# Kernel optimization log

Hardware: AMD Instinct MI355X
Metric: run time of the kernel (lower is better)

## Reference

```python
import jax, jax.numpy as jnp
import numpy as np

B, S, IN, OUT = 4, 2048, 4096, 4096


def setup_inputs() -> dict:
    key = jax.random.key(0)
    kx, kw, kb = jax.random.split(key, 3)
    x = jax.random.randint(kx, (B, S, IN), -127, 128, dtype=jnp.int8)
    weight = jax.random.randint(kw, (OUT, IN), -127, 128, dtype=jnp.int8)
    # original module initializes bias to zeros(int32); use random int32 to exercise the add
    bias = jax.random.randint(kb, (1, OUT), -1000, 1000, dtype=jnp.int32)
    return {"x": x, "weight": weight, "bias": bias}


def reference(x, weight, bias):
    x_shape = x.shape
    x2 = x.reshape(-1, x_shape[-1])  # [tokens, IN], int8
    # dot_general with preferred_element_type=int32 -> int8 inputs, int32 accumulate
    y = jax.lax.dot_general(
        x2, weight,
        dimension_numbers=(((1,), (1,)), ((), ())),
        preferred_element_type=jnp.int32,
    )  # [tokens, OUT] int32
    y = y + bias  # broadcast [1, OUT] int32
    return y.reshape(*x_shape[:-1], -1)
```

## Files before the change

### kernel.cpp

```cpp
#include <hip/hip_runtime.h>
#include <stdint.h>

#define M_TOT 8192
#define N_TOT 4096
#define K_TOT 4096

typedef int v4i  __attribute__((ext_vector_type(4)));
typedef int v16i __attribute__((ext_vector_type(16)));

__device__ __forceinline__ void gload_lds16(const void* g, void* l) {
    __builtin_amdgcn_global_load_lds(
        (const __attribute__((address_space(1))) unsigned int*)g,
        (__attribute__((address_space(3))) unsigned int*)l,
        16, 0, 0);
}

#define WAIT_V0_L0() __builtin_amdgcn_s_waitcnt(0x0070)
#define WAIT_V0()    __builtin_amdgcn_s_waitcnt(0x0f70)
#define SBAR()       __builtin_amdgcn_s_barrier()
#define SFENCE()     __builtin_amdgcn_sched_barrier(0)

__global__ __launch_bounds__(256) void pack2(
        const int4* __restrict__ xs, int4* __restrict__ xd,
        const int4* __restrict__ ws, int4* __restrict__ wd) {
    const int t = blockIdx.x * 256 + threadIdx.x;
#pragma unroll
    for (int it = 0; it < 6; ++it) {
        const long g = (long)it * 524288 + t;
        const int4* __restrict__ src = (it < 4) ? xs : ws;
        int4* __restrict__ dst       = (it < 4) ? xd : wd;
        const long o = (it < 4) ? g : g - 2097152;
        int4 r;
        int* rp = (int*)&r;
#pragma unroll
        for (int q = 0; q < 4; ++q) {
            const int4 a = src[o * 4 + q];
            rp[q] = (a.x & 255) | ((a.y & 255) << 8) |
                    ((a.z & 255) << 16) | (a.w << 24);
        }
        dst[o] = r;
    }
}

__global__ __launch_bounds__(512, 2) void i8gemm_bias(
        const signed char* __restrict__ x,
        const signed char* __restrict__ w,
        const int* __restrict__ bias,
        int* __restrict__ out) {
    __shared__ __align__(16) signed char la[2][256 * 128];
    __shared__ __align__(16) signed char lb[2][256 * 128];

    const int tid  = threadIdx.x;
    const int lane = tid & 63;
    const int wv   = tid >> 6;
    const int l31  = lane & 31;
    const int kh   = lane >> 5;
    const int wr   = wv >> 2;
    const int wc   = wv & 3;

    const int flat = blockIdx.y * gridDim.x + blockIdx.x;
    const int swz  = (flat & 7) * 64 + (flat >> 3);
    const int bn0  = (swz & 15) * 256;
    const int bm0  = (swz >> 4) * 256;

    int bv[2];
#pragma unroll
    for (int j = 0; j < 2; ++j) bv[j] = bias[bn0 + wc * 64 + j * 32 + l31];
    v16i acc[4][2];
#pragma unroll
    for (int i = 0; i < 4; ++i)
#pragma unroll
        for (int j = 0; j < 2; ++j)
#pragma unroll
            for (int r = 0; r < 16; ++r) acc[i][j][r] = bv[j];

    const int fc = (lane & 7) ^ ((lane >> 3) & 7);
    const signed char* pa = x + (long)(bm0 + wv * 32 + (lane >> 3)) * K_TOT + fc * 16;
    const signed char* pb = w + (long)(bn0 + wv * 32 + (lane >> 3)) * K_TOT + fc * 16;
    const int sdst = wv * 32 * 128;

    const int swr  = l31 & 7;
    const int aoff = (wr * 128 + l31) * 128;
    const int boff = (wc * 64  + l31) * 128;
    const int cs0 = ((0 + kh) ^ swr) * 16;
    const int cs1 = ((2 + kh) ^ swr) * 16;
    const int cs2 = ((4 + kh) ^ swr) * 16;
    const int cs3 = ((6 + kh) ^ swr) * 16;

    signed char* A0 = &la[0][0]; signed char* A1 = &la[1][0];
    signed char* B0 = &lb[0][0]; signed char* B1 = &lb[1][0];

#pragma unroll
    for (int u = 0; u < 4; ++u) {
        gload_lds16(pa + (long)u * 8 * K_TOT, A0 + sdst + u * 1024);
        gload_lds16(pb + (long)u * 8 * K_TOT, B0 + sdst + u * 1024);
    }
    WAIT_V0();
    SBAR();
    SFENCE();

    v4i a0[4], b0[2], a1[4], b1[2];
#pragma unroll
    for (int i = 0; i < 4; ++i) a0[i] = *(const v4i*)(A0 + aoff + i * 4096 + cs0);
#pragma unroll
    for (int j = 0; j < 2; ++j) b0[j] = *(const v4i*)(B0 + boff + j * 4096 + cs0);

    const int NT = K_TOT / 128;
    for (int kt = 0; kt < NT; ++kt) {
        SFENCE();
        if (kt + 1 < NT) {
            const long k0 = (long)(kt + 1) * 128;
#pragma unroll
            for (int u = 0; u < 4; ++u) {
                gload_lds16(pa + k0 + (long)u * 8 * K_TOT, A1 + sdst + u * 1024);
                gload_lds16(pb + k0 + (long)u * 8 * K_TOT, B1 + sdst + u * 1024);
            }
        }
        SFENCE();
#pragma unroll
        for (int i = 0; i < 4; ++i) a1[i] = *(const v4i*)(A0 + aoff + i * 4096 + cs1);
#pragma unroll
        for (int j = 0; j < 2; ++j) b1[j] = *(const v4i*)(B0 + boff + j * 4096 + cs1);
        SFENCE();
        __builtin_amdgcn_s_setprio(1);
#pragma unroll
        for (int i = 0; i < 4; ++i)
#pragma unroll
            for (int j = 0; j < 2; ++j)
                acc[i][j] = __builtin_amdgcn_mfma_i32_32x32x32_i8(
                    a0[i], b0[j], acc[i][j], 0, 0, 0);
        __builtin_amdgcn_s_setprio(0);
        SFENCE();
#pragma unroll
        for (int i = 0; i < 4; ++i) a0[i] = *(const v4i*)(A0 + aoff + i * 4096 + cs2);
#pragma unroll
        for (int j = 0; j < 2; ++j) b0[j] = *(const v4i*)(B0 + boff + j * 4096 + cs2);
        SFENCE();
        __builtin_amdgcn_s_setprio(1);
#pragma unroll
        for (int i = 0; i < 4; ++i)
#pragma unroll
            for (int j = 0; j < 2; ++j)
                acc[i][j] = __builtin_amdgcn_mfma_i32_32x32x32_i8(
                    a1[i], b1[j], acc[i][j], 0, 0, 0);
        __builtin_amdgcn_s_setprio(0);
        SFENCE();
#pragma unroll
        for (int i = 0; i < 4; ++i) a1[i] = *(const v4i*)(A0 + aoff + i * 4096 + cs3);
#pragma unroll
        for (int j = 0; j < 2; ++j) b1[j] = *(const v4i*)(B0 + boff + j * 4096 + cs3);
        SFENCE();
        __builtin_amdgcn_s_setprio(1);
#pragma unroll
        for (int i = 0; i < 4; ++i)
#pragma unroll
            for (int j = 0; j < 2; ++j)
                acc[i][j] = __builtin_amdgcn_mfma_i32_32x32x32_i8(
                    a0[i], b0[j], acc[i][j], 0, 0, 0);
        __builtin_amdgcn_s_setprio(0);
        SFENCE();
        WAIT_V0_L0();
        SFENCE();
        SBAR();
        SFENCE();
        if (kt + 1 < NT) {
#pragma unroll
            for (int i = 0; i < 4; ++i) a0[i] = *(const v4i*)(A1 + aoff + i * 4096 + cs0);
#pragma unroll
            for (int j = 0; j < 2; ++j) b0[j] = *(const v4i*)(B1 + boff + j * 4096 + cs0);
        }
        SFENCE();
        __builtin_amdgcn_s_setprio(1);
#pragma unroll
        for (int i = 0; i < 4; ++i)
#pragma unroll
            for (int j = 0; j < 2; ++j)
                acc[i][j] = __builtin_amdgcn_mfma_i32_32x32x32_i8(
                    a1[i], b1[j], acc[i][j], 0, 0, 0);
        __builtin_amdgcn_s_setprio(0);

        signed char* t;
        t = A0; A0 = A1; A1 = t;
        t = B0; B0 = B1; B1 = t;
    }

#pragma unroll
    for (int i = 0; i < 4; ++i) {
        const int mbase = bm0 + wr * 128 + i * 32 + 4 * kh;
#pragma unroll
        for (int j = 0; j < 2; ++j) {
            const int n = bn0 + wc * 64 + j * 32 + l31;
#pragma unroll
            for (int r = 0; r < 16; ++r) {
                const int m = mbase + (r & 3) + 8 * (r >> 2);
                out[(long)m * N_TOT + n] = acc[i][j][r];
            }
        }
    }
}

extern "C" void kernel_launch(void* const* d_in, const int* in_sizes, int n_in,
                              void* d_out, int out_size, void* d_ws, size_t ws_size,
                              hipStream_t stream) {
    const int* x32  = (const int*)d_in[0];
    const int* w32  = (const int*)d_in[1];
    const int* bias = (const int*)d_in[2];
    int*       out  = (int*)d_out;

    signed char* xp = (signed char*)d_ws;
    signed char* wp = (signed char*)d_ws + (size_t)M_TOT * K_TOT;

    pack2<<<2048, 256, 0, stream>>>((const int4*)x32, (int4*)xp,
                                    (const int4*)w32, (int4*)wp);

    dim3 grid(N_TOT / 256, M_TOT / 256);
    i8gemm_bias<<<grid, 512, 0, stream>>>(xp, wp, bias, out);
}
```

Before: 390.5 us.

## Load B operand directly from global into registers, bypassing LDS

The weight (B) tile is no longer staged through shared memory. Each wave now loads its B fragments straight from global memory into registers, prefetched one k-tile ahead, while A keeps the double-buffered LDS path. This halves LDS use and removes the LDS writes and reads for B, which could allow more blocks per CU. The cost is duplicated global/L2 reads of B across waves, less coalesced per-row loads, and more vector registers held live. The vmcnt waits are adjusted so that only the A LDS loads are waited on before the barrier.

Result: slower. 427.8 us (+9.5%).

```diff
diff --git a/kernel.cpp b/kernel.cpp
--- a/kernel.cpp
+++ b/kernel.cpp
@@ -15,8 +15,9 @@
         16, 0, 0);
 }
 
+#define WAIT_V6_L0() __builtin_amdgcn_s_waitcnt(0x0076)
 #define WAIT_V0_L0() __builtin_amdgcn_s_waitcnt(0x0070)
-#define WAIT_V0()    __builtin_amdgcn_s_waitcnt(0x0f70)
+#define WAIT_V8()    __builtin_amdgcn_s_waitcnt(0x0f78)
 #define SBAR()       __builtin_amdgcn_s_barrier()
 #define SFENCE()     __builtin_amdgcn_sched_barrier(0)
 
@@ -48,7 +49,6 @@
         const int* __restrict__ bias,
         int* __restrict__ out) {
     __shared__ __align__(16) signed char la[2][256 * 128];
-    __shared__ __align__(16) signed char lb[2][256 * 128];
 
     const int tid  = threadIdx.x;
     const int lane = tid & 63;
@@ -76,34 +76,38 @@
 
     const int fc = (lane & 7) ^ ((lane >> 3) & 7);
     const signed char* pa = x + (long)(bm0 + wv * 32 + (lane >> 3)) * K_TOT + fc * 16;
-    const signed char* pb = w + (long)(bn0 + wv * 32 + (lane >> 3)) * K_TOT + fc * 16;
     const int sdst = wv * 32 * 128;
 
     const int swr  = l31 & 7;
     const int aoff = (wr * 128 + l31) * 128;
-    const int boff = (wc * 64  + l31) * 128;
     const int cs0 = ((0 + kh) ^ swr) * 16;
     const int cs1 = ((2 + kh) ^ swr) * 16;
     const int cs2 = ((4 + kh) ^ swr) * 16;
     const int cs3 = ((6 + kh) ^ swr) * 16;
 
+    const signed char* qb0 = w + (long)(bn0 + wc * 64 + l31) * K_TOT + kh * 16;
+    const signed char* qb1 = qb0 + (long)32 * K_TOT;
+
     signed char* A0 = &la[0][0]; signed char* A1 = &la[1][0];
-    signed char* B0 = &lb[0][0]; signed char* B1 = &lb[1][0];
-
-#pragma unroll
-    for (int u = 0; u < 4; ++u) {
+
+#pragma unroll
+    for (int u = 0; u < 4; ++u)
         gload_lds16(pa + (long)u * 8 * K_TOT, A0 + sdst + u * 1024);
-        gload_lds16(pb + (long)u * 8 * K_TOT, B0 + sdst + u * 1024);
-    }
-    WAIT_V0();
+    SFENCE();
+    v4i b0[2], b1[2], b2[2], b3[2];
+    b0[0] = *(const v4i*)(qb0);      b0[1] = *(const v4i*)(qb1);
+    b1[0] = *(const v4i*)(qb0 + 32); b1[1] = *(const v4i*)(qb1 + 32);
+    b2[0] = *(const v4i*)(qb0 + 64); b2[1] = *(const v4i*)(qb1 + 64);
+    b3[0] = *(const v4i*)(qb0 + 96); b3[1] = *(const v4i*)(qb1 + 96);
+    qb0 += 128; qb1 += 128;
+    SFENCE();
+    WAIT_V8();
     SBAR();
     SFENCE();
 
-    v4i a0[4], b0[2], a1[4], b1[2];
+    v4i a0[4], a1[4];
 #pragma unroll
     for (int i = 0; i < 4; ++i) a0[i] = *(const v4i*)(A0 + aoff + i * 4096 + cs0);
-#pragma unroll
-    for (int j = 0; j < 2; ++j) b0[j] = *(const v4i*)(B0 + boff + j * 4096 + cs0);
 
     const int NT = K_TOT / 128;
     for (int kt = 0; kt < NT; ++kt) {
@@ -111,16 +115,12 @@
         if (kt + 1 < NT) {
             const long k0 = (long)(kt + 1) * 128;
 #pragma unroll
-            for (int u = 0; u < 4; ++u) {
+            for (int u = 0; u < 4; ++u)
                 gload_lds16(pa + k0 + (long)u * 8 * K_TOT, A1 + sdst + u * 1024);
-                gload_lds16(pb + k0 + (long)u * 8 * K_TOT, B1 + sdst + u * 1024);
-            }
         }
         SFENCE();
 #pragma unroll
         for (int i = 0; i < 4; ++i) a1[i] = *(const v4i*)(A0 + aoff + i * 4096 + cs1);
-#pragma unroll
-        for (int j = 0; j < 2; ++j) b1[j] = *(const v4i*)(B0 + boff + j * 4096 + cs1);
         SFENCE();
         __builtin_amdgcn_s_setprio(1);
 #pragma unroll
@@ -133,8 +133,6 @@
         SFENCE();
 #pragma unroll
         for (int i = 0; i < 4; ++i) a0[i] = *(const v4i*)(A0 + aoff + i * 4096 + cs2);
-#pragma unroll
-        for (int j = 0; j < 2; ++j) b0[j] = *(const v4i*)(B0 + boff + j * 4096 + cs2);
         SFENCE();
         __builtin_amdgcn_s_setprio(1);
 #pragma unroll
@@ -145,43 +143,51 @@
                     a1[i], b1[j], acc[i][j], 0, 0, 0);
         __builtin_amdgcn_s_setprio(0);
         SFENCE();
+        if (kt + 1 < NT) {
+            b0[0] = *(const v4i*)(qb0);      b0[1] = *(const v4i*)(qb1);
+            b1[0] = *(const v4i*)(qb0 + 32); b1[1] = *(const v4i*)(qb1 + 32);
+        }
+        SFENCE();
 #pragma unroll
         for (int i = 0; i < 4; ++i) a1[i] = *(const v4i*)(A0 + aoff + i * 4096 + cs3);
-#pragma unroll
-        for (int j = 0; j < 2; ++j) b1[j] = *(const v4i*)(B0 + boff + j * 4096 + cs3);
-        SFENCE();
-        __builtin_amdgcn_s_setprio(1);
-#pragma unroll
-        for (int i = 0; i < 4; ++i)
-#pragma unroll
-            for (int j = 0; j < 2; ++j)
-                acc[i][j] = __builtin_amdgcn_mfma_i32_32x32x32_i8(
-                    a0[i], b0[j], acc[i][j], 0, 0, 0);
-        __builtin_amdgcn_s_setprio(0);
-        SFENCE();
-        WAIT_V0_L0();
+        SFENCE();
+        __builtin_amdgcn_s_setprio(1);
+#pragma unroll
+        for (int i = 0; i < 4; ++i)
+#pragma unroll
+            for (int j = 0; j < 2; ++j)
+                acc[i][j] = __builtin_amdgcn_mfma_i32_32x32x32_i8(
+                    a0[i], b2[j], acc[i][j], 0, 0, 0);
+        __builtin_amdgcn_s_setprio(0);
+        SFENCE();
+        if (kt + 1 < NT) {
+            b2[0] = *(const v4i*)(qb0 + 64); b2[1] = *(const v4i*)(qb1 + 64);
+        }
+        SFENCE();
+        if (kt + 1 < NT) { WAIT_V6_L0(); } else { WAIT_V0_L0(); }
         SFENCE();
         SBAR();
         SFENCE();
         if (kt + 1 < NT) {
 #pragma unroll
             for (int i = 0; i < 4; ++i) a0[i] = *(const v4i*)(A1 + aoff + i * 4096 + cs0);
-#pragma unroll
-            for (int j = 0; j < 2; ++j) b0[j] = *(const v4i*)(B1 + boff + j * 4096 + cs0);
-        }
-        SFENCE();
-        __builtin_amdgcn_s_setprio(1);
-#pragma unroll
-        for (int i = 0; i < 4; ++i)
-#pragma unroll
-            for (int j = 0; j < 2; ++j)
-                acc[i][j] = __builtin_amdgcn_mfma_i32_32x32x32_i8(
-                    a1[i], b1[j], acc[i][j], 0, 0, 0);
-        __builtin_amdgcn_s_setprio(0);
-
-        signed char* t;
-        t = A0; A0 = A1; A1 = t;
-        t = B0; B0 = B1; B1 = t;
+        }
+        SFENCE();
+        __builtin_amdgcn_s_setprio(1);
+#pragma unroll
+        for (int i = 0; i < 4; ++i)
+#pragma unroll
+            for (int j = 0; j < 2; ++j)
+                acc[i][j] = __builtin_amdgcn_mfma_i32_32x32x32_i8(
+                    a1[i], b3[j], acc[i][j], 0, 0, 0);
+        __builtin_amdgcn_s_setprio(0);
+        SFENCE();
+        if (kt + 1 < NT) {
+            b3[0] = *(const v4i*)(qb0 + 96); b3[1] = *(const v4i*)(qb1 + 96);
+            qb0 += 128; qb1 += 128;
+        }
+
+        signed char* t = A0; A0 = A1; A1 = t;
     }
 
 #pragma unroll
```
